# Kernel tuning notes

Measured on AMD Instinct MI355X. Metric: run time of the kernel, lower is better.

The kernel has to match this reference:

```python
import jax, jax.numpy as jnp
import numpy as np

N_NODES = 50000
N_EDGES = 1600000  # even; edges come in reverse pairs (i, i^1)
D_NODE = 128
D_EDGE = 32
UNITS = 128
STEPS = 4


def setup_inputs() -> dict:
    key = jax.random.key(0)
    ks = jax.random.split(key, 8)
    # Build directed edges as adjacent reverse pairs so rev(e) = e XOR 1.
    half = N_EDGES // 2
    src = jax.random.randint(ks[0], (half,), 0, N_NODES, dtype=jnp.int32)
    dst = jax.random.randint(ks[1], (half,), 0, N_NODES, dtype=jnp.int32)
    edge_src = jnp.stack([src, dst], axis=1).reshape(-1)
    edge_dst = jnp.stack([dst, src], axis=1).reshape(-1)
    node_feature = jax.random.normal(ks[2], (N_NODES, D_NODE), dtype=jnp.float32)
    edge_feature = jax.random.normal(ks[3], (N_EDGES, D_EDGE), dtype=jnp.float32)
    s_i = 1.0 / np.sqrt(D_NODE + D_EDGE)
    s_u = 1.0 / np.sqrt(UNITS)
    s_f = 1.0 / np.sqrt(D_NODE + UNITS)
    Wi = jax.random.normal(ks[4], (D_NODE + D_EDGE, UNITS), dtype=jnp.float32) * s_i
    Wu = jax.random.normal(ks[5], (UNITS, UNITS), dtype=jnp.float32) * s_u
    Wf = jax.random.normal(ks[6], (D_NODE + UNITS, UNITS), dtype=jnp.float32) * s_f
    bi = jnp.zeros((UNITS,), jnp.float32)
    bu = jnp.zeros((UNITS,), jnp.float32)
    bf = jnp.zeros((UNITS,), jnp.float32)
    return {
        'node_feature': node_feature, 'edge_feature': edge_feature,
        'edge_src': edge_src, 'edge_dst': edge_dst,
        'Wi': Wi, 'bi': bi, 'Wu': Wu, 'bu': bu, 'Wf': Wf, 'bf': bf,
    }


def reference(node_feature, edge_feature, edge_src, edge_dst, Wi, bi, Wu, bu, Wf, bf):
    n_nodes = node_feature.shape[0]
    n_edges = edge_src.shape[0]
    # reverse edge of e is e XOR 1 (edges built as adjacent pairs)
    rev = jnp.bitwise_xor(jnp.arange(n_edges, dtype=jnp.int32), 1)

    # initial projection: relu([x_src || e] Wi + bi)  -> [E, UNITS]
    h = jax.nn.relu(
        jnp.concatenate([node_feature[edge_src], edge_feature], axis=-1) @ Wi + bi)

    for _ in range(STEPS):
        # aggregate incoming edge states at each node, gather at edge_src,
        # subtract the reverse edge state (DMPNN message)
        agg = jax.ops.segment_sum(h, edge_dst, num_segments=n_nodes)  # [N, UNITS]
        message = agg[edge_src] - h[rev]                              # [E, UNITS]
        h = jax.nn.relu(message @ Wu + bu + h)

    node_message = jax.ops.segment_sum(h, edge_dst, num_segments=n_nodes)
    out = jax.nn.relu(
        jnp.concatenate([node_feature, node_message], axis=-1) @ Wf + bf)
    return out
```

## Files before the change

### kernel.cpp

```cpp
#include <hip/hip_runtime.h>
#include <hip/hip_bf16.h>

#define N_NODES 50000
#define N_EDGES 1600000
#define TILE    128

typedef __bf16 bf16x8 __attribute__((ext_vector_type(8)));
typedef float  f32x4  __attribute__((ext_vector_type(4)));

static __device__ __forceinline__ bf16x8 ld8(const __bf16* p) {
  return *reinterpret_cast<const bf16x8*>(p);
}
static __device__ __forceinline__ void st8(__bf16* p, bf16x8 v) {
  *reinterpret_cast<bf16x8*>(p) = v;
}

static __device__ __forceinline__ void async16(const void* g, void* l) {
  auto gp = (const __attribute__((address_space(1))) unsigned int*)(unsigned long long)g;
  auto lp = (__attribute__((address_space(3))) unsigned int*)(unsigned int)(unsigned long long)l;
  __builtin_amdgcn_global_load_lds(gp, lp, 16, 0, 0);
}

__global__ __launch_bounds__(256) void k_prep_w(
    const float* __restrict__ Wi, const float* __restrict__ Wu,
    const float* __restrict__ Wf,
    __bf16* __restrict__ WiT, __bf16* __restrict__ WuT, __bf16* __restrict__ WfT)
{
  int g = blockIdx.x * 256 + threadIdx.x;
  if (g < 160 * 128) {
    int n = g / 160, k = g % 160;
    WiT[g] = (__bf16)Wi[k * 128 + n];
  } else if (g < 160 * 128 + 128 * 128) {
    int gg = g - 160 * 128;
    int n = gg / 128, k = gg % 128;
    WuT[gg] = (__bf16)Wu[k * 128 + n];
  } else if (g < 160 * 128 + 128 * 128 + 256 * 128) {
    int gg = g - (160 * 128 + 128 * 128);
    int n = gg / 256, k = gg % 256;
    WfT[gg] = (__bf16)Wf[k * 128 + n];
  }
}

__global__ __launch_bounds__(256) void k_cvt(
    const float* __restrict__ in, __bf16* __restrict__ out, long n)
{
  long i = ((long)blockIdx.x * 256 + threadIdx.x) * 8;
  if (i + 8 <= n) {
    f32x4 f0 = *(const f32x4*)(in + i);
    f32x4 f1 = *(const f32x4*)(in + i + 4);
    bf16x8 o;
#pragma unroll
    for (int j = 0; j < 4; ++j) { o[j] = (__bf16)f0[j]; o[4 + j] = (__bf16)f1[j]; }
    st8(out + i, o);
  }
}

__global__ __launch_bounds__(256) void k_hist(
    const int* __restrict__ edst, int* __restrict__ cnt)
{
  int e = blockIdx.x * 256 + threadIdx.x;
  if (e < N_EDGES) atomicAdd(&cnt[edst[e]], 1);
}

__global__ __launch_bounds__(1024) void k_scan1(
    int* __restrict__ cnt, int* __restrict__ bsum, int n)
{
  __shared__ int sm[1024];
  const int tid = threadIdx.x;
  int i = blockIdx.x * 1024 + tid;
  int v = (i < n) ? cnt[i] : 0;
  sm[tid] = v;
  __syncthreads();
  for (int off = 1; off < 1024; off <<= 1) {
    int t = (tid >= off) ? sm[tid - off] : 0;
    __syncthreads();
    sm[tid] += t;
    __syncthreads();
  }
  if (i < n) cnt[i] = sm[tid] - v;
  if (tid == 1023) bsum[blockIdx.x] = sm[1023];
}

__global__ __launch_bounds__(64) void k_scan2(int* __restrict__ bsum, int nb)
{
  if (threadIdx.x == 0) {
    int acc = 0;
    for (int k = 0; k < nb; ++k) { int t = bsum[k]; bsum[k] = acc; acc += t; }
  }
}

__global__ __launch_bounds__(256) void k_scan3(
    const int* __restrict__ cnt, const int* __restrict__ bsum,
    int* __restrict__ cursor, int n)
{
  int i = blockIdx.x * 256 + threadIdx.x;
  if (i < n) cursor[i] = cnt[i] + bsum[i >> 10];
}

__global__ __launch_bounds__(256) void k_fill(
    const int* __restrict__ edst, int* __restrict__ cursor, int* __restrict__ eidx)
{
  int e = blockIdx.x * 256 + threadIdx.x;
  if (e < N_EDGES) {
    int p = atomicAdd(&cursor[edst[e]], 1);
    eidx[p] = e;
  }
}

__global__ __launch_bounds__(256) void k_agg(
    const __bf16* __restrict__ h, const int* __restrict__ cnt,
    const int* __restrict__ bsum, const int* __restrict__ eidx,
    __bf16* __restrict__ aggbf)
{
  const int wave = threadIdx.x >> 6;
  const int node = blockIdx.x * 4 + wave;
  const int lane = threadIdx.x & 63;
  const int g = lane >> 4, c16 = lane & 15;
  const int s = cnt[node] + bsum[node >> 10];
  const int e = (node + 1 < N_NODES) ? (cnt[node + 1] + bsum[(node + 1) >> 10]) : N_EDGES;
  const int deg = e - s;

  float a[8] = {0.f, 0.f, 0.f, 0.f, 0.f, 0.f, 0.f, 0.f};
  if (deg > 0) {
    const int* bucket = eidx + s;
    const int nit = (deg + 3) >> 2;
    int j = g;
    int ecur = bucket[(j < deg) ? j : 0];
    bool vcur = (j < deg);
    for (int it = 0; it < nit; ++it) {
      int jn = j + 4;
      int enext = bucket[(jn < deg) ? jn : 0];
      bf16x8 v = ld8(h + (long)ecur * 128 + c16 * 8);
#pragma unroll
      for (int k = 0; k < 8; ++k) a[k] += vcur ? (float)v[k] : 0.f;
      ecur = enext; vcur = (jn < deg); j = jn;
    }
  }
#pragma unroll
  for (int k = 0; k < 8; ++k) {
    a[k] += __shfl_xor(a[k], 16, 64);
    a[k] += __shfl_xor(a[k], 32, 64);
  }
  if (g == 0) {
    bf16x8 o;
#pragma unroll
    for (int k = 0; k < 8; ++k) o[k] = (__bf16)a[k];
    st8(aggbf + (long)node * 128 + c16 * 8, o);
  }
}

__global__ __launch_bounds__(256) void k_nodegemm(
    const __bf16* __restrict__ A, const __bf16* __restrict__ BT, const int ldb,
    const float* __restrict__ bias, float* __restrict__ outf, const int nrows)
{
  const int tid = threadIdx.x;
  const int lane = tid & 63, wave = tid >> 6;
  const int l15 = lane & 15, quad = lane >> 4;
  const int wm = wave >> 1, wn = wave & 1;
  const int base = blockIdx.x * TILE;

  int rowm[4];
#pragma unroll
  for (int ms = 0; ms < 4; ++ms) {
    int nd = base + wm * 64 + ms * 16 + l15;
    rowm[ms] = nd < nrows ? nd : (nrows - 1);
  }
  f32x4 acc[4][4] = {};
#pragma unroll
  for (int kit = 0; kit < 4; ++kit) {
    const int koff = kit * 32 + quad * 8;
    bf16x8 a[4];
#pragma unroll
    for (int ms = 0; ms < 4; ++ms)
      a[ms] = ld8(A + (long)rowm[ms] * 128 + koff);
#pragma unroll
    for (int ns = 0; ns < 4; ++ns) {
      bf16x8 b = ld8(BT + (wn * 64 + ns * 16 + l15) * ldb + koff);
#pragma unroll
      for (int ms = 0; ms < 4; ++ms)
        acc[ms][ns] = __builtin_amdgcn_mfma_f32_16x16x32_bf16(a[ms], b, acc[ms][ns], 0, 0, 0);
    }
  }
#pragma unroll
  for (int ns = 0; ns < 4; ++ns) {
    const int col = wn * 64 + ns * 16 + l15;
    const float bv = bias[col];
#pragma unroll
    for (int ms = 0; ms < 4; ++ms) {
      const int r0 = wm * 64 + ms * 16 + quad * 4;
#pragma unroll
      for (int r = 0; r < 4; ++r) {
        const int node = base + r0 + r;
        if (node < nrows) outf[(long)node * 128 + col] = acc[ms][ns][r] + bv;
      }
    }
  }
}

__global__ __launch_bounds__(256) void k_init(
    const float* __restrict__ ef, const int* __restrict__ esrc,
    const __bf16* __restrict__ WiT, const float* __restrict__ q,
    __bf16* __restrict__ h)
{
  __shared__ __align__(16) char smem[32768];
  float*  efT  = (float*)smem;
  __bf16* cbuf = (__bf16*)smem;
  const int tid = threadIdx.x;
  const int lane = tid & 63, wave = tid >> 6;
  const int l15 = lane & 15, quad = lane >> 4;
  const int wm = wave >> 1, wn = wave & 1;
  const long base = (long)blockIdx.x * TILE;

#pragma unroll
  for (int j = 0; j < 4; ++j) {
    const int r = wave * 32 + j * 8 + (lane >> 3);
    const int cd = (lane & 7) ^ (r & 7);
    async16(ef + (base + r) * 32 + cd * 4, efT + (wave * 32 + j * 8) * 32);
  }
  __syncthreads();

  f32x4 acc[4][4] = {};
  {
    bf16x8 a[4];
#pragma unroll
    for (int ms = 0; ms < 4; ++ms) {
      const int rm = wm * 64 + ms * 16 + l15;
      const int c0 = (quad * 2) ^ (rm & 7);
      f32x4 f0 = *(const f32x4*)(efT + rm * 32 + c0 * 4);
      f32x4 f1 = *(const f32x4*)(efT + rm * 32 + (c0 ^ 1) * 4);
      bf16x8 v;
#pragma unroll
      for (int j = 0; j < 4; ++j) { v[j] = (__bf16)f0[j]; v[4 + j] = (__bf16)f1[j]; }
      a[ms] = v;
    }
#pragma unroll
    for (int ns = 0; ns < 4; ++ns) {
      bf16x8 b = ld8(WiT + (wn * 64 + ns * 16 + l15) * 160 + 128 + quad * 8);
#pragma unroll
      for (int ms = 0; ms < 4; ++ms)
        acc[ms][ns] = __builtin_amdgcn_mfma_f32_16x16x32_bf16(a[ms], b, acc[ms][ns], 0, 0, 0);
    }
  }

  const int c15 = tid & 15, rbase = tid >> 4;
  int srcv[8];
#pragma unroll
  for (int i = 0; i < 8; ++i) srcv[i] = esrc[base + i * 16 + rbase];

  __syncthreads();
#pragma unroll
  for (int ns = 0; ns < 4; ++ns) {
    const int col = wn * 64 + ns * 16 + l15;
#pragma unroll
    for (int ms = 0; ms < 4; ++ms) {
      const int r0 = wm * 64 + ms * 16 + quad * 4;
#pragma unroll
      for (int r = 0; r < 4; ++r) {
        const int row = r0 + r;
        cbuf[row * 128 + (((col >> 3) ^ (row & 15)) * 8) + (col & 7)] = (__bf16)acc[ms][ns][r];
      }
    }
  }
  __syncthreads();

  f32x4 g0 = *(const f32x4*)(q + (long)srcv[0] * 128 + c15 * 8);
  f32x4 g1 = *(const f32x4*)(q + (long)srcv[0] * 128 + c15 * 8 + 4);
#pragma unroll
  for (int i = 0; i < 8; ++i) {
    f32x4 ng0, ng1;
    if (i < 7) {
      const float* gp = q + (long)srcv[i + 1] * 128 + c15 * 8;
      ng0 = *(const f32x4*)gp; ng1 = *(const f32x4*)(gp + 4);
    }
    const int row = i * 16 + rbase;
    bf16x8 cv = ld8(cbuf + row * 128 + ((c15 ^ (row & 15)) * 8));
    bf16x8 o;
#pragma unroll
    for (int j = 0; j < 8; ++j) {
      float gj = (j < 4) ? g0[j] : g1[j - 4];
      float v = gj + (float)cv[j];
      v = v > 0.f ? v : 0.f;
      o[j] = (__bf16)v;
    }
    st8(h + (base + row) * 128 + c15 * 8, o);
    g0 = ng0; g1 = ng1;
  }
}

__global__ __launch_bounds__(256) void k_update(
    __bf16* __restrict__ h, const int* __restrict__ esrc,
    const __bf16* __restrict__ WuT, const float* __restrict__ gW)
{
  __shared__ __align__(16) __bf16 smem[128 * 128];
  const int tid = threadIdx.x;
  const int lane = tid & 63, wave = tid >> 6;
  const int l15 = lane & 15, quad = lane >> 4;
  const int wm = wave >> 1, wn = wave & 1;
  const long base = (long)blockIdx.x * TILE;

#pragma unroll
  for (int j = 0; j < 8; ++j) {
    const int r = wave * 32 + j * 4 + (lane >> 4);
    const int cd = (lane & 15) ^ (r & 15);
    async16(h + (base + r) * 128 + cd * 8, smem + (wave * 32 + j * 4) * 128);
  }
  __syncthreads();

  f32x4 acc[4][4] = {};
#pragma unroll
  for (int kit = 0; kit < 4; ++kit) {
    bf16x8 a[4];
#pragma unroll
    for (int ms = 0; ms < 4; ++ms) {
      const int rm = wm * 64 + ms * 16 + l15;
      a[ms] = ld8(smem + rm * 128 + (((kit * 4 + quad) ^ l15) * 8));
    }
#pragma unroll
    for (int ns = 0; ns < 4; ++ns) {
      bf16x8 b = ld8(WuT + (wn * 64 + ns * 16 + l15) * 128 + kit * 32 + quad * 8);
#pragma unroll
      for (int ms = 0; ms < 4; ++ms)
        acc[ms][ns] = __builtin_amdgcn_mfma_f32_16x16x32_bf16(a[ms], b, acc[ms][ns], 0, 0, 0);
    }
  }

  const int c15 = tid & 15, rbase = tid >> 4;
  bf16x8 hv[8];
  int srcv[8];
#pragma unroll
  for (int i = 0; i < 8; ++i) {
    const int row = i * 16 + rbase;
    hv[i] = ld8(smem + row * 128 + ((c15 ^ (row & 15)) * 8));
    srcv[i] = esrc[base + row];
  }
  __syncthreads();
#pragma unroll
  for (int ns = 0; ns < 4; ++ns) {
    const int col = wn * 64 + ns * 16 + l15;
#pragma unroll
    for (int ms = 0; ms < 4; ++ms) {
      const int r0 = wm * 64 + ms * 16 + quad * 4;
#pragma unroll
      for (int r = 0; r < 4; ++r) {
        const int row = r0 + r;
        smem[row * 128 + (((col >> 3) ^ (row & 15)) * 8) + (col & 7)] = (__bf16)acc[ms][ns][r];
      }
    }
  }
  __syncthreads();

  f32x4 g0 = *(const f32x4*)(gW + (long)srcv[0] * 128 + c15 * 8);
  f32x4 g1 = *(const f32x4*)(gW + (long)srcv[0] * 128 + c15 * 8 + 4);
#pragma unroll
  for (int i = 0; i < 8; ++i) {
    f32x4 ng0, ng1;
    if (i < 7) {
      const float* gp = gW + (long)srcv[i + 1] * 128 + c15 * 8;
      ng0 = *(const f32x4*)gp; ng1 = *(const f32x4*)(gp + 4);
    }
    const int row = i * 16 + rbase;
    const int rowr = row ^ 1;
    bf16x8 cv = ld8(smem + rowr * 128 + ((c15 ^ (rowr & 15)) * 8));
    bf16x8 o;
#pragma unroll
    for (int j = 0; j < 8; ++j) {
      float gj = (j < 4) ? g0[j] : g1[j - 4];
      float v = gj - (float)cv[j] + (float)hv[i][j];
      v = v > 0.f ? v : 0.f;
      o[j] = (__bf16)v;
    }
    st8(h + (base + row) * 128 + c15 * 8, o);
    g0 = ng0; g1 = ng1;
  }
}

__global__ __launch_bounds__(256) void k_final(
    const __bf16* __restrict__ nfbf, const __bf16* __restrict__ aggbf,
    const __bf16* __restrict__ WfT, const float* __restrict__ bfb,
    float* __restrict__ out)
{
  const int tid = threadIdx.x;
  const int lane = tid & 63, wave = tid >> 6;
  const int l15 = lane & 15, quad = lane >> 4;
  const int wm = wave >> 1, wn = wave & 1;
  const int base = blockIdx.x * TILE;

  int nodem[4];
#pragma unroll
  for (int ms = 0; ms < 4; ++ms) {
    int nd = base + wm * 64 + ms * 16 + l15;
    nodem[ms] = nd < N_NODES ? nd : (N_NODES - 1);
  }
  f32x4 acc[4][4] = {};
#pragma unroll
  for (int kit = 0; kit < 8; ++kit) {
    const int koff = kit * 32 + quad * 8;
    bf16x8 a[4];
#pragma unroll
    for (int ms = 0; ms < 4; ++ms)
      a[ms] = (kit < 4) ? ld8(nfbf + (long)nodem[ms] * 128 + koff)
                        : ld8(aggbf + (long)nodem[ms] * 128 + (koff - 128));
#pragma unroll
    for (int ns = 0; ns < 4; ++ns) {
      bf16x8 b = ld8(WfT + (wn * 64 + ns * 16 + l15) * 256 + koff);
#pragma unroll
      for (int ms = 0; ms < 4; ++ms)
        acc[ms][ns] = __builtin_amdgcn_mfma_f32_16x16x32_bf16(a[ms], b, acc[ms][ns], 0, 0, 0);
    }
  }
#pragma unroll
  for (int ns = 0; ns < 4; ++ns) {
    const int col = wn * 64 + ns * 16 + l15;
    const float bias = bfb[col];
#pragma unroll
    for (int ms = 0; ms < 4; ++ms) {
      const int r0 = wm * 64 + ms * 16 + quad * 4;
#pragma unroll
      for (int r = 0; r < 4; ++r) {
        const int node = base + r0 + r;
        if (node < N_NODES) {
          float v = acc[ms][ns][r] + bias;
          out[(long)node * 128 + col] = v > 0.f ? v : 0.f;
        }
      }
    }
  }
}

extern "C" void kernel_launch(void* const* d_in, const int* in_sizes, int n_in,
                              void* d_out, int out_size, void* d_ws, size_t ws_size,
                              hipStream_t stream) {
  const float* nf   = (const float*)d_in[0];
  const float* ef   = (const float*)d_in[1];
  const int*   esrc = (const int*)d_in[2];
  const int*   edst = (const int*)d_in[3];
  const float* Wi   = (const float*)d_in[4];
  const float* bi   = (const float*)d_in[5];
  const float* Wu   = (const float*)d_in[6];
  const float* bu   = (const float*)d_in[7];
  const float* Wf   = (const float*)d_in[8];
  const float* bfb  = (const float*)d_in[9];
  float* out = (float*)d_out;

  char* ws = (char*)d_ws;
  __bf16* h      = (__bf16*)(ws);
  __bf16* aggbf  = (__bf16*)(ws + 409600000L);
  __bf16* nfbf   = (__bf16*)(ws + 422400000L);
  __bf16* WiT    = (__bf16*)(ws + 435200000L);
  __bf16* WuT    = (__bf16*)(ws + 435240960L);
  __bf16* WfT    = (__bf16*)(ws + 435273728L);
  int*    cnt    = (int*)(ws + 435339264L);
  int*    cursor = (int*)(ws + 435539264L);
  int*    bsum   = (int*)(ws + 435739264L);
  int*    eidx   = (int*)(ws + 435739520L);
  float*  g      = (float*)(ws + 442139520L);

  const long NV = (long)N_NODES * 128;
  const int  NGB = (N_NODES + TILE - 1) / TILE;

  hipLaunchKernelGGL(k_prep_w, dim3(272), dim3(256), 0, stream, Wi, Wu, Wf, WiT, WuT, WfT);
  hipLaunchKernelGGL(k_cvt, dim3(3125), dim3(256), 0, stream, nf, nfbf, NV);
  hipMemsetAsync(cnt, 0, 200000, stream);
  hipLaunchKernelGGL(k_hist, dim3(N_EDGES / 256), dim3(256), 0, stream, edst, cnt);
  hipLaunchKernelGGL(k_scan1, dim3(49), dim3(1024), 0, stream, cnt, bsum, N_NODES);
  hipLaunchKernelGGL(k_scan2, dim3(1), dim3(64), 0, stream, bsum, 49);
  hipLaunchKernelGGL(k_scan3, dim3(196), dim3(256), 0, stream, cnt, bsum, cursor, N_NODES);
  hipLaunchKernelGGL(k_fill, dim3(N_EDGES / 256), dim3(256), 0, stream, edst, cursor, eidx);

  hipLaunchKernelGGL(k_nodegemm, dim3(NGB), dim3(256), 0, stream, nfbf, WiT, 160, bi, g, N_NODES);
  hipLaunchKernelGGL(k_init, dim3(N_EDGES / TILE), dim3(256), 0, stream, ef, esrc, WiT, g, h);

  for (int t = 0; t < 4; ++t) {
    hipLaunchKernelGGL(k_agg, dim3(N_NODES / 4), dim3(256), 0, stream, h, cnt, bsum, eidx, aggbf);
    hipLaunchKernelGGL(k_nodegemm, dim3(NGB), dim3(256), 0, stream, aggbf, WuT, 128, bu, g, N_NODES);
    hipLaunchKernelGGL(k_update, dim3(N_EDGES / TILE), dim3(256), 0, stream, h, esrc, WuT, g);
  }
  hipLaunchKernelGGL(k_agg, dim3(N_NODES / 4), dim3(256), 0, stream, h, cnt, bsum, eidx, aggbf);
  hipLaunchKernelGGL(k_final, dim3(NGB), dim3(256), 0, stream, nfbf, aggbf, WfT, bfb, out);
}
```

Measured before the change: 2.415 ms.

## Store per-node projections in bf16 and widen edge gather in aggregation

The per-node GEMM output g, which is gathered per edge in the init and update kernels, is now stored as bf16 instead of fp32. This halves the random-gather traffic, and the gather is prefetched two rows ahead instead of one. The aggregation kernel now has 8 lanes cover a 256-byte row (32 bytes per lane), processes 8 edges per iteration and keeps a deeper index prefetch. The cost is an extra rounding of g to bf16, which adds some precision loss.

```diff
diff --git a/kernel.cpp b/kernel.cpp
--- a/kernel.cpp
+++ b/kernel.cpp
@@ -115,43 +115,52 @@
   const int wave = threadIdx.x >> 6;
   const int node = blockIdx.x * 4 + wave;
   const int lane = threadIdx.x & 63;
-  const int g = lane >> 4, c16 = lane & 15;
+  const int g = lane >> 3, c8 = lane & 7;
   const int s = cnt[node] + bsum[node >> 10];
   const int e = (node + 1 < N_NODES) ? (cnt[node + 1] + bsum[(node + 1) >> 10]) : N_EDGES;
   const int deg = e - s;
 
-  float a[8] = {0.f, 0.f, 0.f, 0.f, 0.f, 0.f, 0.f, 0.f};
+  float a[16] = {};
   if (deg > 0) {
     const int* bucket = eidx + s;
-    const int nit = (deg + 3) >> 2;
-    int j = g;
-    int ecur = bucket[(j < deg) ? j : 0];
-    bool vcur = (j < deg);
+    const int nit = (deg + 7) >> 3;
+    int j0 = g;
+    int e0 = bucket[(j0 < deg) ? j0 : 0];
+    int e1 = bucket[(j0 + 8 < deg) ? j0 + 8 : 0];
+    bool v0 = (j0 < deg), v1 = (j0 + 8 < deg);
     for (int it = 0; it < nit; ++it) {
-      int jn = j + 4;
-      int enext = bucket[(jn < deg) ? jn : 0];
-      bf16x8 v = ld8(h + (long)ecur * 128 + c16 * 8);
-#pragma unroll
-      for (int k = 0; k < 8; ++k) a[k] += vcur ? (float)v[k] : 0.f;
-      ecur = enext; vcur = (jn < deg); j = jn;
-    }
-  }
-#pragma unroll
-  for (int k = 0; k < 8; ++k) {
+      const int j2 = j0 + 16;
+      const int e2 = bucket[(j2 < deg) ? j2 : 0];
+      const __bf16* hp = h + (long)e0 * 128 + c8 * 16;
+      bf16x8 r0 = ld8(hp), r1 = ld8(hp + 8);
+#pragma unroll
+      for (int k = 0; k < 8; ++k) {
+        a[k]     += v0 ? (float)r0[k] : 0.f;
+        a[8 + k] += v0 ? (float)r1[k] : 0.f;
+      }
+      e0 = e1; v0 = v1;
+      e1 = e2; v1 = (j2 < deg);
+      j0 += 8;
+    }
+  }
+#pragma unroll
+  for (int k = 0; k < 16; ++k) {
+    a[k] += __shfl_xor(a[k], 8, 64);
     a[k] += __shfl_xor(a[k], 16, 64);
     a[k] += __shfl_xor(a[k], 32, 64);
   }
   if (g == 0) {
-    bf16x8 o;
-#pragma unroll
-    for (int k = 0; k < 8; ++k) o[k] = (__bf16)a[k];
-    st8(aggbf + (long)node * 128 + c16 * 8, o);
+    bf16x8 o0, o1;
+#pragma unroll
+    for (int k = 0; k < 8; ++k) { o0[k] = (__bf16)a[k]; o1[k] = (__bf16)a[8 + k]; }
+    st8(aggbf + (long)node * 128 + c8 * 16, o0);
+    st8(aggbf + (long)node * 128 + c8 * 16 + 8, o1);
   }
 }
 
 __global__ __launch_bounds__(256) void k_nodegemm(
     const __bf16* __restrict__ A, const __bf16* __restrict__ BT, const int ldb,
-    const float* __restrict__ bias, float* __restrict__ outf, const int nrows)
+    const float* __restrict__ bias, __bf16* __restrict__ outb, const int nrows)
 {
   const int tid = threadIdx.x;
   const int lane = tid & 63, wave = tid >> 6;
@@ -191,7 +200,7 @@
 #pragma unroll
       for (int r = 0; r < 4; ++r) {
         const int node = base + r0 + r;
-        if (node < nrows) outf[(long)node * 128 + col] = acc[ms][ns][r] + bv;
+        if (node < nrows) outb[(long)node * 128 + col] = (__bf16)(acc[ms][ns][r] + bv);
       }
     }
   }
@@ -199,7 +208,7 @@
 
 __global__ __launch_bounds__(256) void k_init(
     const float* __restrict__ ef, const int* __restrict__ esrc,
-    const __bf16* __restrict__ WiT, const float* __restrict__ q,
+    const __bf16* __restrict__ WiT, const __bf16* __restrict__ q,
     __bf16* __restrict__ h)
 {
   __shared__ __align__(16) char smem[32768];
@@ -246,6 +255,8 @@
   int srcv[8];
 #pragma unroll
   for (int i = 0; i < 8; ++i) srcv[i] = esrc[base + i * 16 + rbase];
+  bf16x8 gp0 = ld8(q + (long)srcv[0] * 128 + c15 * 8);
+  bf16x8 gp1 = ld8(q + (long)srcv[1] * 128 + c15 * 8);
 
   __syncthreads();
 #pragma unroll
@@ -263,33 +274,27 @@
   }
   __syncthreads();
 
-  f32x4 g0 = *(const f32x4*)(q + (long)srcv[0] * 128 + c15 * 8);
-  f32x4 g1 = *(const f32x4*)(q + (long)srcv[0] * 128 + c15 * 8 + 4);
 #pragma unroll
   for (int i = 0; i < 8; ++i) {
-    f32x4 ng0, ng1;
-    if (i < 7) {
-      const float* gp = q + (long)srcv[i + 1] * 128 + c15 * 8;
-      ng0 = *(const f32x4*)gp; ng1 = *(const f32x4*)(gp + 4);
-    }
+    bf16x8 gnext;
+    if (i < 6) gnext = ld8(q + (long)srcv[i + 2] * 128 + c15 * 8);
     const int row = i * 16 + rbase;
     bf16x8 cv = ld8(cbuf + row * 128 + ((c15 ^ (row & 15)) * 8));
     bf16x8 o;
 #pragma unroll
     for (int j = 0; j < 8; ++j) {
-      float gj = (j < 4) ? g0[j] : g1[j - 4];
-      float v = gj + (float)cv[j];
+      float v = (float)gp0[j] + (float)cv[j];
       v = v > 0.f ? v : 0.f;
       o[j] = (__bf16)v;
     }
     st8(h + (base + row) * 128 + c15 * 8, o);
-    g0 = ng0; g1 = ng1;
+    gp0 = gp1; gp1 = gnext;
   }
 }
 
 __global__ __launch_bounds__(256) void k_update(
     __bf16* __restrict__ h, const int* __restrict__ esrc,
-    const __bf16* __restrict__ WuT, const float* __restrict__ gW)
+    const __bf16* __restrict__ WuT, const __bf16* __restrict__ gW)
 {
   __shared__ __align__(16) __bf16 smem[128 * 128];
   const int tid = threadIdx.x;
@@ -333,6 +338,9 @@
     hv[i] = ld8(smem + row * 128 + ((c15 ^ (row & 15)) * 8));
     srcv[i] = esrc[base + row];
   }
+  bf16x8 gp0 = ld8(gW + (long)srcv[0] * 128 + c15 * 8);
+  bf16x8 gp1 = ld8(gW + (long)srcv[1] * 128 + c15 * 8);
+
   __syncthreads();
 #pragma unroll
   for (int ns = 0; ns < 4; ++ns) {
@@ -349,28 +357,22 @@
   }
   __syncthreads();
 
-  f32x4 g0 = *(const f32x4*)(gW + (long)srcv[0] * 128 + c15 * 8);
-  f32x4 g1 = *(const f32x4*)(gW + (long)srcv[0] * 128 + c15 * 8 + 4);
 #pragma unroll
   for (int i = 0; i < 8; ++i) {
-    f32x4 ng0, ng1;
-    if (i < 7) {
-      const float* gp = gW + (long)srcv[i + 1] * 128 + c15 * 8;
-      ng0 = *(const f32x4*)gp; ng1 = *(const f32x4*)(gp + 4);
-    }
+    bf16x8 gnext;
+    if (i < 6) gnext = ld8(gW + (long)srcv[i + 2] * 128 + c15 * 8);
     const int row = i * 16 + rbase;
     const int rowr = row ^ 1;
     bf16x8 cv = ld8(smem + rowr * 128 + ((c15 ^ (rowr & 15)) * 8));
     bf16x8 o;
 #pragma unroll
     for (int j = 0; j < 8; ++j) {
-      float gj = (j < 4) ? g0[j] : g1[j - 4];
-      float v = gj - (float)cv[j] + (float)hv[i][j];
+      float v = (float)gp0[j] - (float)cv[j] + (float)hv[i][j];
       v = v > 0.f ? v : 0.f;
       o[j] = (__bf16)v;
     }
     st8(h + (base + row) * 128 + c15 * 8, o);
-    g0 = ng0; g1 = ng1;
+    gp0 = gp1; gp1 = gnext;
   }
 }
 
@@ -453,7 +455,7 @@
   int*    cursor = (int*)(ws + 435539264L);
   int*    bsum   = (int*)(ws + 435739264L);
   int*    eidx   = (int*)(ws + 435739520L);
-  float*  g      = (float*)(ws + 442139520L);
+  __bf16* g      = (__bf16*)(ws + 442139520L);
 
   const long NV = (long)N_NODES * 128;
   const int  NGB = (N_NODES + TILE - 1) / TILE;
```

Measured after the change: 2.175 ms. 9.9% less time.
